# Kernel optimization log

Measured on AMD Instinct MI355X. Metric: run time of the kernel, lower is better.

Reference implementation:

```python
import jax, jax.numpy as jnp
import numpy as np

B, N, E, NF, G, H, R, L = 64, 50000, 300000, 128, 256, 512, 3, 2


def setup_inputs() -> dict:
    key = jax.random.key(0)
    ks = jax.random.split(key, 24)
    s = 0.02
    inp = {
        # CodeBERT CLS embedding (encoder treated as external pretrained module)
        "cls": jax.random.normal(ks[0], (B, 768), jnp.float32),
        "nf": jax.random.normal(ks[1], (N, NF), jnp.float32),
        "ei": jax.random.randint(ks[2], (2, E), 0, N, dtype=jnp.int32),
        "et": jax.random.randint(ks[3], (E,), 0, R, dtype=jnp.int32),
        "bv": jnp.sort(jax.random.randint(ks[4], (N,), 0, B, dtype=jnp.int32)),
        # node_proj: Linear(128, 256)
        "node_w": jax.random.normal(ks[5], (NF, G), jnp.float32) * s,
        "node_b": jnp.zeros((G,), jnp.float32),
        # RGCN layers: per-layer [R] relation weights (no bias) + self-loop Linear
        "rel_w": jax.random.normal(ks[6], (L, R, G, G), jnp.float32) * s,
        "self_w": jax.random.normal(ks[7], (L, G, G), jnp.float32) * s,
        "self_b": jnp.zeros((L, G), jnp.float32),
        # text_proj: Linear(768, 512)
        "text_w": jax.random.normal(ks[8], (768, H), jnp.float32) * s,
        "text_b": jnp.zeros((H,), jnp.float32),
        # graph_proj: Linear(256, 512)
        "graph_w": jax.random.normal(ks[9], (G, H), jnp.float32) * s,
        "graph_b": jnp.zeros((H,), jnp.float32),
        # GatedFusion gate: Linear(1024, 512)
        "gate_w": jax.random.normal(ks[10], (2 * H, H), jnp.float32) * s,
        "gate_b": jnp.zeros((H,), jnp.float32),
        # classifier: Linear(512,256) -> ReLU -> Linear(256,2) (dropout = eval identity)
        "c1_w": jax.random.normal(ks[11], (H, H // 2), jnp.float32) * s,
        "c1_b": jnp.zeros((H // 2,), jnp.float32),
        "c2_w": jax.random.normal(ks[12], (H // 2, 2), jnp.float32) * s,
        "c2_b": jnp.zeros((2,), jnp.float32),
    }
    return inp


def reference(cls, nf, ei, et, bv, node_w, node_b, rel_w, self_w, self_b,
              text_w, text_b, graph_w, graph_b, gate_w, gate_b,
              c1_w, c1_b, c2_w, c2_b):
    h = cls @ text_w + text_b                      # [B, H]
    x = nf @ node_w + node_b                       # [N, G]
    src, dst = ei[0], ei[1]
    n_nodes = x.shape[0]
    n_layers, n_rel = rel_w.shape[0], rel_w.shape[1]
    for l in range(n_layers):
        out = x @ self_w[l] + self_b[l]            # self-loop
        xs = x[src]                                # gather [E, G]
        for r in range(n_rel):
            msg = jnp.where((et == r)[:, None], xs @ rel_w[l, r], 0.0)
            out = out + jax.ops.segment_sum(msg, dst, num_segments=n_nodes)
        x = jax.nn.relu(out)
    n_graphs = cls.shape[0]
    hg = jax.ops.segment_sum(x, bv, num_segments=n_graphs)          # [B, G]
    cnt = jax.ops.segment_sum(jnp.ones((n_nodes,), x.dtype), bv, num_segments=n_graphs)
    hg = (hg / jnp.maximum(cnt, 1.0)[:, None]) @ graph_w + graph_b  # [B, H]
    g = jax.nn.sigmoid(jnp.concatenate([h, hg], axis=-1) @ gate_w + gate_b)
    f = g * h + (1.0 - g) * hg
    z = jax.nn.relu(f @ c1_w + c1_b)
    return z @ c2_w + c2_b                          # [B, 2] logits
```

## Files before the change

### kernel.cpp

```cpp
#include <hip/hip_runtime.h>
#include <hip/hip_bf16.h>
#include <cstdint>
#include <cstddef>

constexpr int GDIM = 256;
constexpr int HDIM = 512;
constexpr int NF   = 128;

typedef __attribute__((ext_vector_type(8))) short bf16x8;
typedef __attribute__((ext_vector_type(4))) float f32x4;

__device__ __forceinline__ unsigned short f2bf(float x) {
  union { float f; unsigned int u; } v; v.f = x;
  unsigned int r = v.u + 0x7FFF + ((v.u >> 16) & 1);
  return (unsigned short)(r >> 16);
}
__device__ __forceinline__ float bf2f(unsigned int h) {
  union { unsigned int u; float f; } v; v.u = h << 16; return v.f;
}

__device__ __forceinline__ void gload16(const void* g, void* l) {
  __builtin_amdgcn_global_load_lds(
      (const __attribute__((address_space(1))) unsigned int*)g,
      (__attribute__((address_space(3))) unsigned int*)l, 16, 0, 0);
}

__global__ __launch_bounds__(256) void mfma_gemm(
    const unsigned short* __restrict__ A, const unsigned short* __restrict__ Wt,
    const float* __restrict__ bias, unsigned short* __restrict__ out,
    int M, int K, int ldout, int nbias, int ncb)
{
  __shared__ __align__(16) unsigned short lds[2 * 128 * 64];
  char* ldsb = (char*)lds;
  const int nwg  = gridDim.x;
  const int orig = blockIdx.x;
  const int q = nwg >> 3, r = nwg & 7;
  const int xcd = orig & 7, sidx = orig >> 3;
  const int wgid = (xcd < r ? xcd * (q + 1) : r * (q + 1) + (xcd - r) * q) + sidx;
  const int row0 = (wgid / ncb) * 128;
  const int n0   = (wgid % ncb) * 128;

  const int t    = threadIdx.x;
  const int lane = t & 63;
  const int w    = t >> 6;
  const int wr   = w >> 1, wc = w & 1;

  f32x4 acc[4][4] = {};

  const int srow  = lane >> 3;
  const int sslot = lane & 7;

  for (int k0 = 0; k0 < K; k0 += 64) {
    __syncthreads();
#pragma unroll
    for (int i = 0; i < 4; ++i) {
      int row  = (i * 4 + w) * 8 + srow;
      int slot = sslot ^ (row & 7);
      int grA  = min(row0 + row, M - 1);
      gload16(A  + (size_t)grA        * K + k0 + slot * 8, ldsb +         (i * 4 + w) * 1024);
      gload16(Wt + (size_t)(n0 + row) * K + k0 + slot * 8, ldsb + 16384 + (i * 4 + w) * 1024);
    }
    __syncthreads();

#pragma unroll
    for (int kc = 0; kc < 2; ++kc) {
      bf16x8 af[4], bfr[4];
#pragma unroll
      for (int m = 0; m < 4; ++m) {
        int row  = wr * 64 + m * 16 + (lane & 15);
        int slot = (kc * 4 + (lane >> 4)) ^ (row & 7);
        af[m] = *(const bf16x8*)(ldsb + row * 128 + slot * 16);
      }
#pragma unroll
      for (int n = 0; n < 4; ++n) {
        int row  = wc * 64 + n * 16 + (lane & 15);
        int slot = (kc * 4 + (lane >> 4)) ^ (row & 7);
        bfr[n] = *(const bf16x8*)(ldsb + 16384 + row * 128 + slot * 16);
      }
#pragma unroll
      for (int m = 0; m < 4; ++m)
#pragma unroll
        for (int n = 0; n < 4; ++n)
          acc[m][n] = __builtin_amdgcn_mfma_f32_16x16x32_bf16(af[m], bfr[n], acc[m][n], 0, 0, 0);
    }
  }

#pragma unroll
  for (int m = 0; m < 4; ++m) {
    int rbase = row0 + wr * 64 + m * 16 + (lane >> 4) * 4;
#pragma unroll
    for (int n = 0; n < 4; ++n) {
      int c = n0 + wc * 64 + n * 16 + (lane & 15);
      float badd = (c < nbias) ? bias[c] : 0.f;
#pragma unroll
      for (int i = 0; i < 4; ++i) {
        int rr = rbase + i;
        if (rr < M) out[(size_t)rr * ldout + c] = f2bf(acc[m][n][i] + badd);
      }
    }
  }
}

__global__ __launch_bounds__(256) void convert_bf16(
    const float* __restrict__ x, unsigned short* __restrict__ xb, int n)
{
  int i = (blockIdx.x * 256 + threadIdx.x) * 4;
  if (i >= n) return;
  float4 v = *(const float4*)(x + i);
  ushort4 o; o.x = f2bf(v.x); o.y = f2bf(v.y); o.z = f2bf(v.z); o.w = f2bf(v.w);
  *(ushort4*)(xb + i) = o;
}

__global__ __launch_bounds__(256) void prep_all(
    const float* __restrict__ node_w, const float* __restrict__ self_w,
    const float* __restrict__ rel_w, unsigned short* __restrict__ wt_node,
    unsigned short* __restrict__ wt_l0, unsigned short* __restrict__ wt_l1)
{
  int idx = blockIdx.x * 256 + threadIdx.x;
  if (idx < 256 * 128) {
    int nn = idx >> 7, kk = idx & 127;
    wt_node[idx] = f2bf(node_w[kk * 256 + nn]);
    return;
  }
  idx -= 256 * 128;
  if (idx >= 8 * 65536) return;
  int region = idx >> 16;
  int rem = idx & 65535;
  int l = region >> 2, m = region & 3;
  int nn = rem >> 8, kk = rem & 255;
  const float* wsrc = (m == 0) ? (self_w + (size_t)l * 65536)
                               : (rel_w + ((size_t)l * 3 + (m - 1)) * 65536);
  unsigned short* wdst = (l ? wt_l1 : wt_l0) + (size_t)m * 65536;
  wdst[rem] = f2bf(wsrc[kk * 256 + nn]);
}

__global__ __launch_bounds__(256) void histo_kernel(
    const int* __restrict__ dst, int* __restrict__ deg, int E)
{
  int e = blockIdx.x * 256 + threadIdx.x;
  if (e < E) atomicAdd(&deg[dst[e]], 1);
}

__global__ __launch_bounds__(256) void scan_partial(
    const int* __restrict__ deg, int* __restrict__ incl, int* __restrict__ bsum, int N)
{
  __shared__ int s[256];
  int t = threadIdx.x;
  int n = blockIdx.x * 256 + t;
  int v = (n < N) ? deg[n] : 0;
  s[t] = v;
  __syncthreads();
#pragma unroll
  for (int o = 1; o < 256; o <<= 1) {
    int u = (t >= o) ? s[t - o] : 0;
    __syncthreads();
    s[t] += u;
    __syncthreads();
  }
  if (n < N) incl[n] = s[t];
  if (t == 255) bsum[blockIdx.x] = s[255];
}

__global__ __launch_bounds__(256) void scan_sums(int* __restrict__ bsum, int nb)
{
  __shared__ int s[256];
  int t = threadIdx.x;
  int v = (t < nb) ? bsum[t] : 0;
  s[t] = v;
  __syncthreads();
#pragma unroll
  for (int o = 1; o < 256; o <<= 1) {
    int u = (t >= o) ? s[t - o] : 0;
    __syncthreads();
    s[t] += u;
    __syncthreads();
  }
  if (t < nb) bsum[t] = s[t] - v;
}

__global__ __launch_bounds__(256) void scan_add(
    const int* __restrict__ incl, const int* __restrict__ deg,
    const int* __restrict__ bsum, int* __restrict__ off, int N, int E)
{
  int n = blockIdx.x * 256 + threadIdx.x;
  if (n < N) off[n] = incl[n] - deg[n] + bsum[n >> 8];
  if (n == 0) off[N] = E;
}

__global__ __launch_bounds__(256) void fill_kernel(
    const int* __restrict__ src, const int* __restrict__ dst,
    const int* __restrict__ et, const int* __restrict__ off,
    int* __restrict__ cursor, int* __restrict__ psrc, int* __restrict__ prel, int E)
{
  int e = blockIdx.x * 256 + threadIdx.x;
  if (e >= E) return;
  int d = dst[e];
  int pos = atomicAdd(&cursor[d], 1);
  int idx = off[d] + pos;
  psrc[idx] = src[e];
  prel[idx] = et[e];
}

__global__ __launch_bounds__(256) void aggregate_kernel(
    const int* __restrict__ off, const int* __restrict__ psrc,
    const int* __restrict__ prel, const unsigned short* __restrict__ yb,
    unsigned short* __restrict__ xout, int N)
{
  int n = blockIdx.x * 4 + (threadIdx.x >> 6);
  if (n >= N) return;
  int lane = threadIdx.x & 63;
  uint2 s = *(const uint2*)(yb + (size_t)n * 1024 + lane * 4);
  float4 acc;
  acc.x = bf2f(s.x & 0xFFFF); acc.y = bf2f(s.x >> 16);
  acc.z = bf2f(s.y & 0xFFFF); acc.w = bf2f(s.y >> 16);
  int i0 = off[n], i1 = off[n + 1];
  for (int i = i0; i < i1; ++i) {
    int sn = psrc[i], rr = prel[i];
    uint2 u = *(const uint2*)(yb + (size_t)sn * 1024 + 256 + rr * 256 + lane * 4);
    acc.x += bf2f(u.x & 0xFFFF); acc.y += bf2f(u.x >> 16);
    acc.z += bf2f(u.y & 0xFFFF); acc.w += bf2f(u.y >> 16);
  }
  ushort4 o;
  o.x = f2bf(fmaxf(acc.x, 0.f)); o.y = f2bf(fmaxf(acc.y, 0.f));
  o.z = f2bf(fmaxf(acc.z, 0.f)); o.w = f2bf(fmaxf(acc.w, 0.f));
  *(ushort4*)(xout + (size_t)n * 256 + lane * 4) = o;
}

__global__ __launch_bounds__(256) void pool_kernel(
    const unsigned short* __restrict__ xb, const int* __restrict__ bv,
    float* __restrict__ hg, float* __restrict__ cnt, int N)
{
  __shared__ int sbv[128];
  int n0 = blockIdx.x * 128;
  int t = threadIdx.x;
  int nmax = min(128, N - n0);
  if (t < nmax) sbv[t] = bv[n0 + t];
  __syncthreads();
  float run = 0.f;
  int cur = sbv[0];
  for (int i = 0; i < nmax; ++i) {
    int b = sbv[i];
    if (b != cur) { atomicAdd(&hg[cur * GDIM + t], run); run = 0.f; cur = b; }
    run += bf2f(xb[(size_t)(n0 + i) * GDIM + t]);
  }
  atomicAdd(&hg[cur * GDIM + t], run);
  if (t == 0) {
    float c = 0.f; int cb = sbv[0];
    for (int i = 0; i < nmax; ++i) {
      int b = sbv[i];
      if (b != cb) { atomicAdd(&cnt[cb], c); c = 0.f; cb = b; }
      c += 1.f;
    }
    atomicAdd(&cnt[cb], c);
  }
}

__global__ __launch_bounds__(256) void smallgemm_partial(
    const float* __restrict__ X, const float* __restrict__ W,
    float* __restrict__ partial, int K, int Ncols, int KC,
    const float* __restrict__ cntp)
{
  int j  = blockIdx.x * 256 + threadIdx.x;
  int b  = blockIdx.y;
  int ks = blockIdx.z;
  if (j >= Ncols) return;
  int k0 = ks * KC, k1 = min(K, k0 + KC);
  const float* xr = X + (size_t)b * K;
  float s0 = 0.f, s1 = 0.f, s2 = 0.f, s3 = 0.f;
  int k = k0;
  for (; k + 4 <= k1; k += 4) {
    s0 = fmaf(xr[k + 0], W[(size_t)(k + 0) * Ncols + j], s0);
    s1 = fmaf(xr[k + 1], W[(size_t)(k + 1) * Ncols + j], s1);
    s2 = fmaf(xr[k + 2], W[(size_t)(k + 2) * Ncols + j], s2);
    s3 = fmaf(xr[k + 3], W[(size_t)(k + 3) * Ncols + j], s3);
  }
  for (; k < k1; ++k) s0 = fmaf(xr[k], W[(size_t)k * Ncols + j], s0);
  float s = (s0 + s1) + (s2 + s3);
  if (cntp) s *= 1.f / fmaxf(cntp[b], 1.f);
  partial[((size_t)ks * gridDim.y + b) * Ncols + j] = s;
}

__global__ __launch_bounds__(256) void ep_sum(
    const float* __restrict__ partial, const float* __restrict__ bias,
    float* __restrict__ out, float* __restrict__ out2,
    int Ncols, int KS, int relu, int ld2, int off2)
{
  int j = blockIdx.x * 256 + threadIdx.x;
  int b = blockIdx.y;
  if (j >= Ncols) return;
  float s = bias ? bias[j] : 0.f;
  for (int ks = 0; ks < KS; ++ks)
    s += partial[((size_t)ks * gridDim.y + b) * Ncols + j];
  if (relu) s = fmaxf(s, 0.f);
  out[(size_t)b * Ncols + j] = s;
  if (out2) out2[(size_t)b * ld2 + off2 + j] = s;
}

__global__ __launch_bounds__(256) void ep_gate(
    const float* __restrict__ partial, const float* __restrict__ gb,
    const float* __restrict__ h, const float* __restrict__ hgp,
    float* __restrict__ f, int KS)
{
  int j = blockIdx.x * 256 + threadIdx.x;
  int b = blockIdx.y;
  float s = gb[j];
  for (int ks = 0; ks < KS; ++ks)
    s += partial[((size_t)ks * gridDim.y + b) * HDIM + j];
  float g = 1.f / (1.f + expf(-s));
  f[(size_t)b * HDIM + j] = g * h[(size_t)b * HDIM + j] + (1.f - g) * hgp[(size_t)b * HDIM + j];
}

__global__ __launch_bounds__(256) void c2_kernel(
    const float* __restrict__ z, const float* __restrict__ w,
    const float* __restrict__ bias, float* __restrict__ out)
{
  __shared__ float r0[256], r1[256];
  int b = blockIdx.x, t = threadIdx.x;
  float zv = z[(size_t)b * 256 + t];
  r0[t] = zv * w[t * 2 + 0];
  r1[t] = zv * w[t * 2 + 1];
  __syncthreads();
  for (int o = 128; o > 0; o >>= 1) {
    if (t < o) { r0[t] += r0[t + o]; r1[t] += r1[t + o]; }
    __syncthreads();
  }
  if (t == 0) {
    out[b * 2 + 0] = r0[0] + bias[0];
    out[b * 2 + 1] = r1[0] + bias[1];
  }
}

extern "C" void kernel_launch(void* const* d_in, const int* in_sizes, int n_in,
                              void* d_out, int out_size, void* d_ws, size_t ws_size,
                              hipStream_t stream)
{
  const float* cls     = (const float*)d_in[0];
  const float* nf      = (const float*)d_in[1];
  const int*   ei      = (const int*)d_in[2];
  const int*   et      = (const int*)d_in[3];
  const int*   bv      = (const int*)d_in[4];
  const float* node_w  = (const float*)d_in[5];
  const float* node_b  = (const float*)d_in[6];
  const float* rel_w   = (const float*)d_in[7];
  const float* self_w  = (const float*)d_in[8];
  const float* self_b  = (const float*)d_in[9];
  const float* text_w  = (const float*)d_in[10];
  const float* text_b  = (const float*)d_in[11];
  const float* graph_w = (const float*)d_in[12];
  const float* graph_b = (const float*)d_in[13];
  const float* gate_w  = (const float*)d_in[14];
  const float* gate_b  = (const float*)d_in[15];
  const float* c1_w    = (const float*)d_in[16];
  const float* c1_b    = (const float*)d_in[17];
  const float* c2_w    = (const float*)d_in[18];
  const float* c2_b    = (const float*)d_in[19];

  const int Bsz = in_sizes[0] / 768;
  const int Nn  = in_sizes[1] / NF;
  const int E   = in_sizes[3];

  const int* src = ei;
  const int* dst = ei + E;

  float* ws = (float*)d_ws;
  size_t off_f = 0;
  unsigned short* yb  = (unsigned short*)(ws + off_f); off_f += (size_t)Nn * 1024 / 2;
  unsigned short* xb1 = (unsigned short*)(ws + off_f); off_f += (size_t)Nn * GDIM / 2;
  unsigned short* xb2 = (unsigned short*)(ws + off_f); off_f += (size_t)Nn * GDIM / 2;
  float* h   = ws + off_f; off_f += (size_t)Bsz * HDIM;
  float* hg  = ws + off_f; off_f += (size_t)Bsz * GDIM;
  float* cnt = ws + off_f; off_f += (size_t)Bsz;
  float* hgp = ws + off_f; off_f += (size_t)Bsz * HDIM;
  float* f   = ws + off_f; off_f += (size_t)Bsz * HDIM;
  float* z   = ws + off_f; off_f += (size_t)Bsz * (HDIM/2);
  float* hcat= ws + off_f; off_f += (size_t)Bsz * 2 * HDIM;
  float* pp  = ws + off_f; off_f += (size_t)8 * Bsz * HDIM;
  unsigned short* wt_node = (unsigned short*)(ws + off_f); off_f += (GDIM * NF) / 2;
  unsigned short* wt_l0   = (unsigned short*)(ws + off_f); off_f += (4 * GDIM * GDIM) / 2;
  unsigned short* wt_l1   = (unsigned short*)(ws + off_f); off_f += (4 * GDIM * GDIM) / 2;
  int* csr_off = (int*)(ws + off_f);
  int* psrc    = csr_off + (Nn + 1);
  int* prel    = psrc + E;
  int* deg    = (int*)yb;
  int* incl   = deg + Nn;
  int* cursor = incl + Nn;
  int* bsum   = cursor + Nn;
  unsigned short* nfb = xb2;

  dim3 blk(256);
  const int nbN = (Nn + 255) / 256;
  const int nbE = (E + 255) / 256;
  const int nrb = (Nn + 127) / 128;
  const int KC  = 128;

  hipMemsetAsync(deg, 0, (size_t)(3 * Nn + 256) * sizeof(int), stream);
  histo_kernel<<<nbE, blk, 0, stream>>>(dst, deg, E);
  scan_partial<<<nbN, blk, 0, stream>>>(deg, incl, bsum, Nn);
  scan_sums<<<1, blk, 0, stream>>>(bsum, nbN);
  scan_add<<<nbN, blk, 0, stream>>>(incl, deg, bsum, csr_off, Nn, E);
  fill_kernel<<<nbE, blk, 0, stream>>>(src, dst, et, csr_off, cursor, psrc, prel, E);

  prep_all<<<(256 * 128 + 8 * 65536 + 255) / 256, blk, 0, stream>>>(
      node_w, self_w, rel_w, wt_node, wt_l0, wt_l1);

  hipMemsetAsync(hg, 0, (size_t)(Bsz * GDIM + Bsz) * sizeof(float), stream);

  smallgemm_partial<<<dim3(2, Bsz, 6), blk, 0, stream>>>(cls, text_w, pp, 768, HDIM, KC, nullptr);
  ep_sum<<<dim3(2, Bsz), blk, 0, stream>>>(pp, text_b, h, hcat, HDIM, 6, 0, 2 * HDIM, 0);

  convert_bf16<<<(Nn * NF) / 4 / 256, blk, 0, stream>>>(nf, nfb, Nn * NF);
  mfma_gemm<<<dim3(nrb * 2), blk, 0, stream>>>(nfb, wt_node, node_b, xb1, Nn, NF, 256, 256, 2);

  mfma_gemm<<<dim3(nrb * 8), blk, 0, stream>>>(xb1, wt_l0, self_b, yb, Nn, GDIM, 1024, 256, 8);
  aggregate_kernel<<<dim3((Nn + 3) / 4), blk, 0, stream>>>(csr_off, psrc, prel, yb, xb2, Nn);

  mfma_gemm<<<dim3(nrb * 8), blk, 0, stream>>>(xb2, wt_l1, self_b + GDIM, yb, Nn, GDIM, 1024, 256, 8);
  aggregate_kernel<<<dim3((Nn + 3) / 4), blk, 0, stream>>>(csr_off, psrc, prel, yb, xb1, Nn);

  pool_kernel<<<dim3((Nn + 127) / 128), blk, 0, stream>>>(xb1, bv, hg, cnt, Nn);

  smallgemm_partial<<<dim3(2, Bsz, 2), blk, 0, stream>>>(hg, graph_w, pp, GDIM, HDIM, KC, cnt);
  ep_sum<<<dim3(2, Bsz), blk, 0, stream>>>(pp, graph_b, hgp, hcat, HDIM, 2, 0, 2 * HDIM, HDIM);

  smallgemm_partial<<<dim3(2, Bsz, 8), blk, 0, stream>>>(hcat, gate_w, pp, 2 * HDIM, HDIM, KC, nullptr);
  ep_gate<<<dim3(2, Bsz), blk, 0, stream>>>(pp, gate_b, h, hgp, f, 8);

  smallgemm_partial<<<dim3(1, Bsz, 4), blk, 0, stream>>>(f, c1_w, pp, HDIM, HDIM / 2, KC, nullptr);
  ep_sum<<<dim3(1, Bsz), blk, 0, stream>>>(pp, c1_b, z, nullptr, HDIM / 2, 4, 1, 0, 0);
  c2_kernel<<<dim3(Bsz), blk, 0, stream>>>(z, c2_w, c2_b, (float*)d_out);
}
```

Before: 528.1 us.

## Aggregate raw features per relation before GEMM and double-buffer MFMA LDS tiles

```diff
diff --git a/kernel.cpp b/kernel.cpp
--- a/kernel.cpp
+++ b/kernel.cpp
@@ -28,17 +28,17 @@
 __global__ __launch_bounds__(256) void mfma_gemm(
     const unsigned short* __restrict__ A, const unsigned short* __restrict__ Wt,
     const float* __restrict__ bias, unsigned short* __restrict__ out,
-    int M, int K, int ldout, int nbias, int ncb)
-{
-  __shared__ __align__(16) unsigned short lds[2 * 128 * 64];
+    int M, int K, int ldout, int relu)
+{
+  __shared__ __align__(16) unsigned short lds[2 * 2 * 128 * 64];
   char* ldsb = (char*)lds;
   const int nwg  = gridDim.x;
   const int orig = blockIdx.x;
   const int q = nwg >> 3, r = nwg & 7;
   const int xcd = orig & 7, sidx = orig >> 3;
   const int wgid = (xcd < r ? xcd * (q + 1) : r * (q + 1) + (xcd - r) * q) + sidx;
-  const int row0 = (wgid / ncb) * 128;
-  const int n0   = (wgid % ncb) * 128;
+  const int row0 = (wgid >> 1) * 128;
+  const int n0   = (wgid & 1) * 128;
 
   const int t    = threadIdx.x;
   const int lane = t & 63;
@@ -50,18 +50,27 @@
   const int srow  = lane >> 3;
   const int sslot = lane & 7;
 
-  for (int k0 = 0; k0 < K; k0 += 64) {
-    __syncthreads();
+  auto stage = [&](int buf, int k0) {
 #pragma unroll
     for (int i = 0; i < 4; ++i) {
       int row  = (i * 4 + w) * 8 + srow;
       int slot = sslot ^ (row & 7);
       int grA  = min(row0 + row, M - 1);
-      gload16(A  + (size_t)grA        * K + k0 + slot * 8, ldsb +         (i * 4 + w) * 1024);
-      gload16(Wt + (size_t)(n0 + row) * K + k0 + slot * 8, ldsb + 16384 + (i * 4 + w) * 1024);
+      gload16(A  + (size_t)grA        * K + k0 + slot * 8,
+              ldsb + buf * 32768 + (i * 4 + w) * 1024);
+      gload16(Wt + (size_t)(n0 + row) * K + k0 + slot * 8,
+              ldsb + buf * 32768 + 16384 + (i * 4 + w) * 1024);
     }
-    __syncthreads();
-
+  };
+
+  stage(0, 0);
+  __syncthreads();
+
+  const int nk = K >> 6;
+  int cur = 0;
+  for (int kt = 0; kt < nk; ++kt) {
+    if (kt + 1 < nk) stage(cur ^ 1, (kt + 1) << 6);
+    char* base = ldsb + cur * 32768;
 #pragma unroll
     for (int kc = 0; kc < 2; ++kc) {
       bf16x8 af[4], bfr[4];
@@ -69,13 +78,13 @@
       for (int m = 0; m < 4; ++m) {
         int row  = wr * 64 + m * 16 + (lane & 15);
         int slot = (kc * 4 + (lane >> 4)) ^ (row & 7);
-        af[m] = *(const bf16x8*)(ldsb + row * 128 + slot * 16);
+        af[m] = *(const bf16x8*)(base + row * 128 + slot * 16);
       }
 #pragma unroll
       for (int n = 0; n < 4; ++n) {
         int row  = wc * 64 + n * 16 + (lane & 15);
         int slot = (kc * 4 + (lane >> 4)) ^ (row & 7);
-        bfr[n] = *(const bf16x8*)(ldsb + 16384 + row * 128 + slot * 16);
+        bfr[n] = *(const bf16x8*)(base + 16384 + row * 128 + slot * 16);
       }
 #pragma unroll
       for (int m = 0; m < 4; ++m)
@@ -83,6 +92,7 @@
         for (int n = 0; n < 4; ++n)
           acc[m][n] = __builtin_amdgcn_mfma_f32_16x16x32_bf16(af[m], bfr[n], acc[m][n], 0, 0, 0);
     }
+    if (kt + 1 < nk) { __syncthreads(); cur ^= 1; }
   }
 
 #pragma unroll
@@ -91,11 +101,15 @@
 #pragma unroll
     for (int n = 0; n < 4; ++n) {
       int c = n0 + wc * 64 + n * 16 + (lane & 15);
-      float badd = (c < nbias) ? bias[c] : 0.f;
+      float badd = bias[c];
 #pragma unroll
       for (int i = 0; i < 4; ++i) {
         int rr = rbase + i;
-        if (rr < M) out[(size_t)rr * ldout + c] = f2bf(acc[m][n][i] + badd);
+        if (rr < M) {
+          float v = acc[m][n][i] + badd;
+          if (relu) v = fmaxf(v, 0.f);
+          out[(size_t)rr * ldout + c] = f2bf(v);
+        }
       }
     }
   }
@@ -123,15 +137,17 @@
     return;
   }
   idx -= 256 * 128;
-  if (idx >= 8 * 65536) return;
-  int region = idx >> 16;
-  int rem = idx & 65535;
-  int l = region >> 2, m = region & 3;
-  int nn = rem >> 8, kk = rem & 255;
-  const float* wsrc = (m == 0) ? (self_w + (size_t)l * 65536)
-                               : (rel_w + ((size_t)l * 3 + (m - 1)) * 65536);
-  unsigned short* wdst = (l ? wt_l1 : wt_l0) + (size_t)m * 65536;
-  wdst[rem] = f2bf(wsrc[kk * 256 + nn]);
+  if (idx >= 2 * 256 * 1024) return;
+  int l = idx >> 18;
+  int rem = idx & 262143;
+  int nn = rem >> 10, k = rem & 1023;
+  float v;
+  if (k < 256) v = self_w[(size_t)l * 65536 + k * 256 + nn];
+  else {
+    int r = (k >> 8) - 1, kk = k & 255;
+    v = rel_w[((size_t)l * 3 + r) * 65536 + kk * 256 + nn];
+  }
+  (l ? wt_l1 : wt_l0)[rem] = f2bf(v);
 }
 
 __global__ __launch_bounds__(256) void histo_kernel(
@@ -203,27 +219,31 @@
 
 __global__ __launch_bounds__(256) void aggregate_kernel(
     const int* __restrict__ off, const int* __restrict__ psrc,
-    const int* __restrict__ prel, const unsigned short* __restrict__ yb,
-    unsigned short* __restrict__ xout, int N)
+    const int* __restrict__ prel, unsigned short* __restrict__ xcat, int N)
 {
   int n = blockIdx.x * 4 + (threadIdx.x >> 6);
   if (n >= N) return;
   int lane = threadIdx.x & 63;
-  uint2 s = *(const uint2*)(yb + (size_t)n * 1024 + lane * 4);
-  float4 acc;
-  acc.x = bf2f(s.x & 0xFFFF); acc.y = bf2f(s.x >> 16);
-  acc.z = bf2f(s.y & 0xFFFF); acc.w = bf2f(s.y >> 16);
+  float4 a0 = {0.f, 0.f, 0.f, 0.f}, a1 = a0, a2 = a0;
   int i0 = off[n], i1 = off[n + 1];
   for (int i = i0; i < i1; ++i) {
     int sn = psrc[i], rr = prel[i];
-    uint2 u = *(const uint2*)(yb + (size_t)sn * 1024 + 256 + rr * 256 + lane * 4);
-    acc.x += bf2f(u.x & 0xFFFF); acc.y += bf2f(u.x >> 16);
-    acc.z += bf2f(u.y & 0xFFFF); acc.w += bf2f(u.y >> 16);
-  }
-  ushort4 o;
-  o.x = f2bf(fmaxf(acc.x, 0.f)); o.y = f2bf(fmaxf(acc.y, 0.f));
-  o.z = f2bf(fmaxf(acc.z, 0.f)); o.w = f2bf(fmaxf(acc.w, 0.f));
-  *(ushort4*)(xout + (size_t)n * 256 + lane * 4) = o;
+    uint2 u = *(const uint2*)(xcat + (size_t)sn * 1024 + lane * 4);
+    float4 v;
+    v.x = bf2f(u.x & 0xFFFF); v.y = bf2f(u.x >> 16);
+    v.z = bf2f(u.y & 0xFFFF); v.w = bf2f(u.y >> 16);
+    if (rr == 0)      { a0.x += v.x; a0.y += v.y; a0.z += v.z; a0.w += v.w; }
+    else if (rr == 1) { a1.x += v.x; a1.y += v.y; a1.z += v.z; a1.w += v.w; }
+    else              { a2.x += v.x; a2.y += v.y; a2.z += v.z; a2.w += v.w; }
+  }
+  unsigned short* o = xcat + (size_t)n * 1024 + 256 + lane * 4;
+  ushort4 s0, s1, s2;
+  s0.x = f2bf(a0.x); s0.y = f2bf(a0.y); s0.z = f2bf(a0.z); s0.w = f2bf(a0.w);
+  s1.x = f2bf(a1.x); s1.y = f2bf(a1.y); s1.z = f2bf(a1.z); s1.w = f2bf(a1.w);
+  s2.x = f2bf(a2.x); s2.y = f2bf(a2.y); s2.z = f2bf(a2.z); s2.w = f2bf(a2.w);
+  *(ushort4*)(o)       = s0;
+  *(ushort4*)(o + 256) = s1;
+  *(ushort4*)(o + 512) = s2;
 }
 
 __global__ __launch_bounds__(256) void pool_kernel(
@@ -364,9 +384,9 @@
 
   float* ws = (float*)d_ws;
   size_t off_f = 0;
-  unsigned short* yb  = (unsigned short*)(ws + off_f); off_f += (size_t)Nn * 1024 / 2;
-  unsigned short* xb1 = (unsigned short*)(ws + off_f); off_f += (size_t)Nn * GDIM / 2;
-  unsigned short* xb2 = (unsigned short*)(ws + off_f); off_f += (size_t)Nn * GDIM / 2;
+  unsigned short* xcat0 = (unsigned short*)(ws + off_f); off_f += (size_t)Nn * 1024 / 2;
+  unsigned short* xcat1 = (unsigned short*)(ws + off_f); off_f += (size_t)Nn * 1024 / 2;
+  unsigned short* xbf   = (unsigned short*)(ws + off_f); off_f += (size_t)Nn * GDIM / 2;
   float* h   = ws + off_f; off_f += (size_t)Bsz * HDIM;
   float* hg  = ws + off_f; off_f += (size_t)Bsz * GDIM;
   float* cnt = ws + off_f; off_f += (size_t)Bsz;
@@ -376,16 +396,16 @@
   float* hcat= ws + off_f; off_f += (size_t)Bsz * 2 * HDIM;
   float* pp  = ws + off_f; off_f += (size_t)8 * Bsz * HDIM;
   unsigned short* wt_node = (unsigned short*)(ws + off_f); off_f += (GDIM * NF) / 2;
-  unsigned short* wt_l0   = (unsigned short*)(ws + off_f); off_f += (4 * GDIM * GDIM) / 2;
-  unsigned short* wt_l1   = (unsigned short*)(ws + off_f); off_f += (4 * GDIM * GDIM) / 2;
+  unsigned short* wt_l0   = (unsigned short*)(ws + off_f); off_f += (GDIM * 1024) / 2;
+  unsigned short* wt_l1   = (unsigned short*)(ws + off_f); off_f += (GDIM * 1024) / 2;
   int* csr_off = (int*)(ws + off_f);
   int* psrc    = csr_off + (Nn + 1);
   int* prel    = psrc + E;
-  int* deg    = (int*)yb;
+  int* deg    = (int*)xcat1;
   int* incl   = deg + Nn;
   int* cursor = incl + Nn;
   int* bsum   = cursor + Nn;
-  unsigned short* nfb = xb2;
+  unsigned short* nfb = (unsigned short*)(cursor + Nn + 256);
 
   dim3 blk(256);
   const int nbN = (Nn + 255) / 256;
@@ -400,7 +420,7 @@
   scan_add<<<nbN, blk, 0, stream>>>(incl, deg, bsum, csr_off, Nn, E);
   fill_kernel<<<nbE, blk, 0, stream>>>(src, dst, et, csr_off, cursor, psrc, prel, E);
 
-  prep_all<<<(256 * 128 + 8 * 65536 + 255) / 256, blk, 0, stream>>>(
+  prep_all<<<(256 * 128 + 2 * 256 * 1024 + 255) / 256, blk, 0, stream>>>(
       node_w, self_w, rel_w, wt_node, wt_l0, wt_l1);
 
   hipMemsetAsync(hg, 0, (size_t)(Bsz * GDIM + Bsz) * sizeof(float), stream);
@@ -409,15 +429,15 @@
   ep_sum<<<dim3(2, Bsz), blk, 0, stream>>>(pp, text_b, h, hcat, HDIM, 6, 0, 2 * HDIM, 0);
 
   convert_bf16<<<(Nn * NF) / 4 / 256, blk, 0, stream>>>(nf, nfb, Nn * NF);
-  mfma_gemm<<<dim3(nrb * 2), blk, 0, stream>>>(nfb, wt_node, node_b, xb1, Nn, NF, 256, 256, 2);
-
-  mfma_gemm<<<dim3(nrb * 8), blk, 0, stream>>>(xb1, wt_l0, self_b, yb, Nn, GDIM, 1024, 256, 8);
-  aggregate_kernel<<<dim3((Nn + 3) / 4), blk, 0, stream>>>(csr_off, psrc, prel, yb, xb2, Nn);
-
-  mfma_gemm<<<dim3(nrb * 8), blk, 0, stream>>>(xb2, wt_l1, self_b + GDIM, yb, Nn, GDIM, 1024, 256, 8);
-  aggregate_kernel<<<dim3((Nn + 3) / 4), blk, 0, stream>>>(csr_off, psrc, prel, yb, xb1, Nn);
-
-  pool_kernel<<<dim3((Nn + 127) / 128), blk, 0, stream>>>(xb1, bv, hg, cnt, Nn);
+  mfma_gemm<<<dim3(nrb * 2), blk, 0, stream>>>(nfb, wt_node, node_b, xcat0, Nn, NF, 1024, 0);
+
+  aggregate_kernel<<<dim3((Nn + 3) / 4), blk, 0, stream>>>(csr_off, psrc, prel, xcat0, Nn);
+  mfma_gemm<<<dim3(nrb * 2), blk, 0, stream>>>(xcat0, wt_l0, self_b, xcat1, Nn, 1024, 1024, 1);
+
+  aggregate_kernel<<<dim3((Nn + 3) / 4), blk, 0, stream>>>(csr_off, psrc, prel, xcat1, Nn);
+  mfma_gemm<<<dim3(nrb * 2), blk, 0, stream>>>(xcat1, wt_l1, self_b + GDIM, xbf, Nn, 1024, 256, 1);
+
+  pool_kernel<<<dim3((Nn + 127) / 128), blk, 0, stream>>>(xbf, bv, hg, cnt, Nn);
 
   smallgemm_partial<<<dim3(2, Bsz, 2), blk, 0, stream>>>(hg, graph_w, pp, GDIM, HDIM, KC, cnt);
   ep_sum<<<dim3(2, Bsz), blk, 0, stream>>>(pp, graph_b, hgp, hcat, HDIM, 2, 0, 2 * HDIM, HDIM);
```

New measurement: 504.8 us. 4.4% less time.
